# Performance work log

Hardware: AMD Instinct MI355X
Metric: run time of the kernel (lower is better)

Reference implementation:

```python
import jax, jax.numpy as jnp
import numpy as np

DIM = 1024
H = 16
DH = DIM // H
THETA = 10000.0


def _rotary_cos_sin(dtype):
    # Faithful to original: rotary is called on q with shape (B, H, 1, DH) and
    # seq_dim=1, so "positions" are t = arange(num_heads).
    inv_freq = 1.0 / (THETA ** (jnp.arange(0, DH, 2, dtype=jnp.float32) / DH))
    t = jnp.arange(H, dtype=jnp.float32)
    freqs = t[:, None] * inv_freq[None, :]          # (H, DH/2)
    emb = jnp.concatenate([freqs, freqs], axis=-1)   # (H, DH)
    cos = jnp.cos(emb)[None, :, None, :].astype(dtype)  # (1, H, 1, DH)
    sin = jnp.sin(emb)[None, :, None, :].astype(dtype)
    return cos, sin


def _rotate_half(x):
    x1, x2 = x[..., : DH // 2], x[..., DH // 2 :]
    return jnp.concatenate([-x2, x1], axis=-1)


def setup_inputs() -> dict:
    key = jax.random.key(0)
    ks = jax.random.split(key, 6)
    B, N = 16, 4096
    s = 1.0 / np.sqrt(DIM)
    return {
        "x": jax.random.normal(ks[0], (B, N, DIM), dtype=jnp.float32),
        "Wq": jax.random.normal(ks[1], (DIM, DIM), dtype=jnp.float32) * s,
        "Wk": jax.random.normal(ks[2], (DIM, DIM), dtype=jnp.float32) * s,
        "Wv": jax.random.normal(ks[3], (DIM, DIM), dtype=jnp.float32) * s,
        "Wp": jax.random.normal(ks[4], (DIM, DIM), dtype=jnp.float32) * s,
        "bp": jax.random.normal(ks[5], (DIM,), dtype=jnp.float32) * 0.01,
    }


def reference(x, Wq, Wk, Wv, Wp, bp):
    B, N, C = x.shape
    scale = DH ** -0.5
    # projections (weights stored as (in, out); x @ W)
    q = (x[:, :1, :] @ Wq).reshape(B, 1, H, DH).transpose(0, 2, 1, 3)  # (B,H,1,DH)
    k = (x @ Wk).reshape(B, N, H, DH).transpose(0, 2, 1, 3)            # (B,H,N,DH)
    v = (x @ Wv).reshape(B, N, H, DH).transpose(0, 2, 1, 3)            # (B,H,N,DH)
    cos, sin = _rotary_cos_sin(x.dtype)
    q = q * cos + _rotate_half(q) * sin
    k = k * cos + _rotate_half(k) * sin  # broadcasts over N (per original)
    attn = jnp.einsum("bhqd,bhkd->bhqk", q, k) * scale  # (B,H,1,N)
    attn = jax.nn.softmax(attn, axis=-1)
    out = jnp.einsum("bhqk,bhkd->bhqd", attn, v)        # (B,H,1,DH)
    out = out.transpose(0, 2, 1, 3).reshape(B, 1, C)
    return out @ Wp + bp
```

## Files before the change

kernel.cpp:

```cpp
#include <hip/hip_runtime.h>

#define NB 16
#define SEQ 4096
#define DIMC 1024
#define NH 16
#define DH 64
#define NC 64
#define RS 16

#define OFF_Q    0
#define OFF_WTIL 16384
#define OFF_PMAX 278528
#define OFF_LC   294912
#define OFF_E    311296
#define OFF_YOUT 1359872
#define OFF_HO   5554176

__global__ __launch_bounds__(256) void kq(const float* __restrict__ x,
                                          const float* __restrict__ Wq,
                                          float* __restrict__ qws) {
  const int jc = blockIdx.x, b = blockIdx.y, t = threadIdx.x;
  const int d = t & 63, g = t >> 6;
  const int j = jc * 64 + d;
  const float* x0 = x + (size_t)b * SEQ * DIMC;
  __shared__ float red[256];
  float a = 0.f;
  #pragma unroll 8
  for (int c = g * 256; c < g * 256 + 256; ++c)
    a = fmaf(x0[c], Wq[(size_t)c * DIMC + j], a);
  red[t] = a;
  __syncthreads();
  if (t < 64)
    qws[b * DIMC + jc * 64 + t] = red[t] + red[64 + t] + red[128 + t] + red[192 + t];
}

__global__ __launch_bounds__(256) void kw(const float* __restrict__ Wk,
                                          const float* __restrict__ qws,
                                          float* __restrict__ wtil) {
  const int cb = blockIdx.x, b = blockIdx.y, t = threadIdx.x;
  const int w = t >> 6, l = t & 63;
  float4 qreg[4];
  {
    const float4* q4 = (const float4*)(qws + b * DIMC + l * 16);
    #pragma unroll
    for (int i = 0; i < 4; ++i) qreg[i] = q4[i];
  }
  const int h = l >> 2;
  float* wt = wtil + ((size_t)b * NH + h) * DIMC;
  #pragma unroll 4
  for (int i = 0; i < 16; ++i) {
    const int c = cb * 64 + w * 16 + i;
    const float4* row = (const float4*)(Wk + (size_t)c * DIMC) + l * 4;
    float s = 0.f;
    #pragma unroll
    for (int k = 0; k < 4; ++k) {
      float4 rv = row[k];
      s = fmaf(rv.x, qreg[k].x, s); s = fmaf(rv.y, qreg[k].y, s);
      s = fmaf(rv.z, qreg[k].z, s); s = fmaf(rv.w, qreg[k].w, s);
    }
    s += __shfl_xor(s, 1);
    s += __shfl_xor(s, 2);
    if ((l & 3) == 0) wt[c] = s * 0.125f;
  }
}

__global__ __launch_bounds__(256) void kS(const float* __restrict__ x,
                                          const float* __restrict__ wtil,
                                          float* __restrict__ e,
                                          float* __restrict__ pmax,
                                          float* __restrict__ Lc) {
  const int nc = blockIdx.x, b = blockIdx.y, t = threadIdx.x;
  const int w = t >> 6, l = t & 63;
  const int wq = __builtin_amdgcn_readfirstlane(w);

  const float4* xrow = (const float4*)x + ((size_t)b * SEQ + nc * 64 + l) * 256 + wq * 64;
  const float4* wt   = (const float4*)wtil + ((size_t)b * NH) * 256 + wq * 64;

  float acc[16] = {0.f, 0.f, 0.f, 0.f, 0.f, 0.f, 0.f, 0.f,
                   0.f, 0.f, 0.f, 0.f, 0.f, 0.f, 0.f, 0.f};
  for (int k4 = 0; k4 < 64; k4 += 4) {
    float4 xv[4];
    #pragma unroll
    for (int i = 0; i < 4; ++i) xv[i] = xrow[k4 + i];
    #pragma unroll
    for (int h = 0; h < 16; ++h) {
      #pragma unroll
      for (int i = 0; i < 4; ++i) {
        float4 wv = wt[h * 256 + k4 + i];
        acc[h] = fmaf(xv[i].x, wv.x, acc[h]);
        acc[h] = fmaf(xv[i].y, wv.y, acc[h]);
        acc[h] = fmaf(xv[i].z, wv.z, acc[h]);
        acc[h] = fmaf(xv[i].w, wv.w, acc[h]);
      }
    }
  }

  __shared__ float4 part[4][4][64];
  #pragma unroll
  for (int q = 0; q < 4; ++q)
    part[q][w][l] = make_float4(acc[4 * q], acc[4 * q + 1], acc[4 * q + 2], acc[4 * q + 3]);
  __syncthreads();

  float4 va;
  {
    float4 p0 = part[w][0][l], p1 = part[w][1][l], p2 = part[w][2][l], p3 = part[w][3][l];
    va.x = (p0.x + p1.x) + (p2.x + p3.x);
    va.y = (p0.y + p1.y) + (p2.y + p3.y);
    va.z = (p0.z + p1.z) + (p2.z + p3.z);
    va.w = (p0.w + p1.w) + (p2.w + p3.w);
  }

  float4 m4 = va;
  #pragma unroll
  for (int o = 1; o < 64; o <<= 1) {
    m4.x = fmaxf(m4.x, __shfl_xor(m4.x, o)); m4.y = fmaxf(m4.y, __shfl_xor(m4.y, o));
    m4.z = fmaxf(m4.z, __shfl_xor(m4.z, o)); m4.w = fmaxf(m4.w, __shfl_xor(m4.w, o));
  }
  float4 pv;
  pv.x = __expf(va.x - m4.x); pv.y = __expf(va.y - m4.y);
  pv.z = __expf(va.z - m4.z); pv.w = __expf(va.w - m4.w);
  float4 s4 = pv;
  #pragma unroll
  for (int o = 1; o < 64; o <<= 1) {
    s4.x += __shfl_xor(s4.x, o); s4.y += __shfl_xor(s4.y, o);
    s4.z += __shfl_xor(s4.z, o); s4.w += __shfl_xor(s4.w, o);
  }
  ((float4*)e)[((size_t)b * SEQ + nc * 64 + l) * 4 + w] = pv;
  if (l == 0) {
    ((float4*)(pmax + ((size_t)b * NC + nc) * NH))[w] = m4;
    ((float4*)(Lc + ((size_t)b * NC + nc) * NH))[w] = s4;
  }
}

__global__ __launch_bounds__(256) void kY(const float* __restrict__ x,
                                          const float* __restrict__ e,
                                          const float* __restrict__ pmax,
                                          const float* __restrict__ Lc,
                                          float* __restrict__ yout) {
  const int rs = blockIdx.x, b = blockIdx.y, t = threadIdx.x;
  __shared__ float4 sc4[NC][4];
  __shared__ float4 pl[64][4];

  if (t < 64) {
    const int ch = t;
    float scl[16];
    #pragma unroll
    for (int h = 0; h < 16; ++h) {
      float m  = pmax[((size_t)b * NC + ch) * NH + h];
      float lc = Lc[((size_t)b * NC + ch) * NH + h];
      float M = m;
      #pragma unroll
      for (int o = 1; o < 64; o <<= 1) M = fmaxf(M, __shfl_xor(M, o));
      float ex = __expf(m - M);
      float lw = lc * ex;
      #pragma unroll
      for (int o = 1; o < 64; o <<= 1) lw += __shfl_xor(lw, o);
      scl[h] = ex / lw;
    }
    #pragma unroll
    for (int q = 0; q < 4; ++q)
      sc4[ch][q] = make_float4(scl[4 * q], scl[4 * q + 1], scl[4 * q + 2], scl[4 * q + 3]);
  }

  const float4* x4 = (const float4*)x + (size_t)b * SEQ * 256;
  const float4* e4 = (const float4*)e + (size_t)b * SEQ * 4;

  float4 acc[16];
  #pragma unroll
  for (int h = 0; h < 16; ++h) acc[h] = make_float4(0.f, 0.f, 0.f, 0.f);

  for (int c4 = 0; c4 < 4; ++c4) {
    const int ch = rs * 4 + c4;
    __syncthreads();
    {
      const int r = t >> 2, qd = t & 3;
      float4 ev = e4[(size_t)(ch * 64 + r) * 4 + qd];
      float4 s  = sc4[ch][qd];
      pl[r][qd] = make_float4(ev.x * s.x, ev.y * s.y, ev.z * s.z, ev.w * s.w);
    }
    __syncthreads();

    const float4* xc = x4 + (size_t)(ch * 64) * 256;
    for (int r = 0; r < 64; r += 2) {
      float4 xva = xc[(size_t)r * 256 + t];
      float4 xvb = xc[(size_t)(r + 1) * 256 + t];
      float4 a0 = pl[r][0], a1 = pl[r][1], a2 = pl[r][2], a3 = pl[r][3];
      float4 b0 = pl[r + 1][0], b1 = pl[r + 1][1], b2 = pl[r + 1][2], b3 = pl[r + 1][3];
      #define ACC(h, ev, xv) acc[h].x = fmaf(ev, xv.x, acc[h].x); acc[h].y = fmaf(ev, xv.y, acc[h].y); \
                             acc[h].z = fmaf(ev, xv.z, acc[h].z); acc[h].w = fmaf(ev, xv.w, acc[h].w)
      ACC(0, a0.x, xva); ACC(1, a0.y, xva); ACC(2, a0.z, xva); ACC(3, a0.w, xva);
      ACC(4, a1.x, xva); ACC(5, a1.y, xva); ACC(6, a1.z, xva); ACC(7, a1.w, xva);
      ACC(8, a2.x, xva); ACC(9, a2.y, xva); ACC(10, a2.z, xva); ACC(11, a2.w, xva);
      ACC(12, a3.x, xva); ACC(13, a3.y, xva); ACC(14, a3.z, xva); ACC(15, a3.w, xva);
      ACC(0, b0.x, xvb); ACC(1, b0.y, xvb); ACC(2, b0.z, xvb); ACC(3, b0.w, xvb);
      ACC(4, b1.x, xvb); ACC(5, b1.y, xvb); ACC(6, b1.z, xvb); ACC(7, b1.w, xvb);
      ACC(8, b2.x, xvb); ACC(9, b2.y, xvb); ACC(10, b2.z, xvb); ACC(11, b2.w, xvb);
      ACC(12, b3.x, xvb); ACC(13, b3.y, xvb); ACC(14, b3.z, xvb); ACC(15, b3.w, xvb);
      #undef ACC
    }
  }

  float4* yo = (float4*)yout + (((size_t)b * RS + rs) * NH) * 256 + t;
  #pragma unroll
  for (int h = 0; h < 16; ++h) yo[h * 256] = acc[h];
}

__global__ __launch_bounds__(256) void kV(const float* __restrict__ yout,
                                          const float* __restrict__ Wv,
                                          float* __restrict__ ho) {
  const int cq = blockIdx.x, h = blockIdx.y, b = blockIdx.z, t = threadIdx.x;
  __shared__ float ysum[DIMC];
  __shared__ float red[256];
  #pragma unroll
  for (int i = 0; i < 4; ++i) {
    const int c = i * 256 + t;
    float s = 0.f;
    #pragma unroll
    for (int r = 0; r < RS; ++r)
      s += yout[(((size_t)b * RS + r) * NH + h) * DIMC + c];
    ysum[c] = s;
  }
  __syncthreads();
  const int d = t & 15, g = t >> 4;
  float a = 0.f;
  #pragma unroll 8
  for (int i = 0; i < 64; ++i)
    a = fmaf(ysum[g * 64 + i], Wv[(size_t)(g * 64 + i) * DIMC + h * DH + cq * 16 + d], a);
  red[t] = a;
  __syncthreads();
  if (t < 16) {
    float s = 0.f;
    #pragma unroll
    for (int j = 0; j < 16; ++j) s += red[j * 16 + t];
    ho[(size_t)b * DIMC + h * DH + cq * 16 + t] = s;
  }
}

__global__ __launch_bounds__(256) void k_out(const float* __restrict__ ho,
                                             const float* __restrict__ Wp,
                                             const float* __restrict__ bp,
                                             float* __restrict__ out) {
  const int jc = blockIdx.x, b = blockIdx.y, t = threadIdx.x;
  __shared__ float hs[1024];
  __shared__ float red[256];
  for (int i = t; i < 1024; i += 256)
    hs[i] = ho[(size_t)b * DIMC + i];
  __syncthreads();
  const int d = t & 63, g = t >> 6;
  const int j = jc * 64 + d;
  float a = 0.f;
  #pragma unroll 8
  for (int i = g * 256; i < g * 256 + 256; ++i)
    a = fmaf(hs[i], Wp[(size_t)i * DIMC + j], a);
  red[t] = a;
  __syncthreads();
  if (t < 64)
    out[(size_t)b * DIMC + jc * 64 + t] =
        red[t] + red[64 + t] + red[128 + t] + red[192 + t] + bp[jc * 64 + t];
}

extern "C" void kernel_launch(void* const* d_in, const int* in_sizes, int n_in,
                              void* d_out, int out_size, void* d_ws, size_t ws_size,
                              hipStream_t stream) {
  const float* x  = (const float*)d_in[0];
  const float* Wq = (const float*)d_in[1];
  const float* Wk = (const float*)d_in[2];
  const float* Wv = (const float*)d_in[3];
  const float* Wp = (const float*)d_in[4];
  const float* bp = (const float*)d_in[5];
  float* out = (float*)d_out;
  float* ws = (float*)d_ws;

  float* qws  = ws + OFF_Q;
  float* wtil = ws + OFF_WTIL;
  float* pmax = ws + OFF_PMAX;
  float* Lc   = ws + OFF_LC;
  float* e    = ws + OFF_E;
  float* yout = ws + OFF_YOUT;
  float* ho   = ws + OFF_HO;

  kq<<<dim3(16, NB), 256, 0, stream>>>(x, Wq, qws);
  kw<<<dim3(16, NB), 256, 0, stream>>>(Wk, qws, wtil);
  kS<<<dim3(NC, NB), 256, 0, stream>>>(x, wtil, e, pmax, Lc);
  kY<<<dim3(RS, NB), 256, 0, stream>>>(x, e, pmax, Lc, yout);
  kV<<<dim3(4, NH, NB), 256, 0, stream>>>(yout, Wv, ho);
  k_out<<<dim3(16, NB), 256, 0, stream>>>(ho, Wp, bp, out);
}
```

Before: 561.0 us.

## Restructure score kernel to per-wave head groups and double row-split count

The score kernel now has each wave hold the reduced weights for four heads in registers and stream rows of x with coalesced float4 loads. Each row's dot product is reduced with wave-wide shuffles, which replaces the old scheme of splitting the channel dimension across waves and combining partials through shared memory. The weighted-sum kernel doubles its row-split count (RS from 16 to 32) so each block handles two chunks instead of four, giving more blocks and more parallelism at the cost of more partial outputs for kV to sum. The inner accumulation loop is unrolled by four rows, and the workspace offset for the head outputs is moved to fit the larger partial buffer.

```diff
diff --git a/kernel.cpp b/kernel.cpp
--- a/kernel.cpp
+++ b/kernel.cpp
@@ -6,7 +6,7 @@
 #define NH 16
 #define DH 64
 #define NC 64
-#define RS 16
+#define RS 32
 
 #define OFF_Q    0
 #define OFF_WTIL 16384
@@ -14,7 +14,7 @@
 #define OFF_LC   294912
 #define OFF_E    311296
 #define OFF_YOUT 1359872
-#define OFF_HO   5554176
+#define OFF_HO   9748480
 
 __global__ __launch_bounds__(256) void kq(const float* __restrict__ x,
                                           const float* __restrict__ Wq,
@@ -64,6 +64,16 @@
   }
 }
 
+__device__ __forceinline__ float dot16(const float4* xv, const float4* wv) {
+  float s = 0.f;
+  #pragma unroll
+  for (int i = 0; i < 4; ++i) {
+    s = fmaf(xv[i].x, wv[i].x, s); s = fmaf(xv[i].y, wv[i].y, s);
+    s = fmaf(xv[i].z, wv[i].z, s); s = fmaf(xv[i].w, wv[i].w, s);
+  }
+  return s;
+}
+
 __global__ __launch_bounds__(256) void kS(const float* __restrict__ x,
                                           const float* __restrict__ wtil,
                                           float* __restrict__ e,
@@ -71,43 +81,36 @@
                                           float* __restrict__ Lc) {
   const int nc = blockIdx.x, b = blockIdx.y, t = threadIdx.x;
   const int w = t >> 6, l = t & 63;
-  const int wq = __builtin_amdgcn_readfirstlane(w);
-
-  const float4* xrow = (const float4*)x + ((size_t)b * SEQ + nc * 64 + l) * 256 + wq * 64;
-  const float4* wt   = (const float4*)wtil + ((size_t)b * NH) * 256 + wq * 64;
-
-  float acc[16] = {0.f, 0.f, 0.f, 0.f, 0.f, 0.f, 0.f, 0.f,
-                   0.f, 0.f, 0.f, 0.f, 0.f, 0.f, 0.f, 0.f};
-  for (int k4 = 0; k4 < 64; k4 += 4) {
-    float4 xv[4];
-    #pragma unroll
-    for (int i = 0; i < 4; ++i) xv[i] = xrow[k4 + i];
-    #pragma unroll
-    for (int h = 0; h < 16; ++h) {
-      #pragma unroll
-      for (int i = 0; i < 4; ++i) {
-        float4 wv = wt[h * 256 + k4 + i];
-        acc[h] = fmaf(xv[i].x, wv.x, acc[h]);
-        acc[h] = fmaf(xv[i].y, wv.y, acc[h]);
-        acc[h] = fmaf(xv[i].z, wv.z, acc[h]);
-        acc[h] = fmaf(xv[i].w, wv.w, acc[h]);
-      }
-    }
-  }
-
-  __shared__ float4 part[4][4][64];
-  #pragma unroll
-  for (int q = 0; q < 4; ++q)
-    part[q][w][l] = make_float4(acc[4 * q], acc[4 * q + 1], acc[4 * q + 2], acc[4 * q + 3]);
-  __syncthreads();
-
-  float4 va;
-  {
-    float4 p0 = part[w][0][l], p1 = part[w][1][l], p2 = part[w][2][l], p3 = part[w][3][l];
-    va.x = (p0.x + p1.x) + (p2.x + p3.x);
-    va.y = (p0.y + p1.y) + (p2.y + p3.y);
-    va.z = (p0.z + p1.z) + (p2.z + p3.z);
-    va.w = (p0.w + p1.w) + (p2.w + p3.w);
+
+  const float4* wt4 = (const float4*)wtil + ((size_t)b * NH + w * 4) * 256;
+  float4 wv[4][4];
+  #pragma unroll
+  for (int h = 0; h < 4; ++h)
+    #pragma unroll
+    for (int i = 0; i < 4; ++i) wv[h][i] = wt4[h * 256 + i * 64 + l];
+  const float4* x4 = (const float4*)x + ((size_t)b * SEQ + nc * 64) * 256;
+  float4 va = make_float4(0.f, 0.f, 0.f, 0.f);
+
+  for (int r = 0; r < 64; r += 2) {
+    float4 xa[4], xb[4];
+    #pragma unroll
+    for (int i = 0; i < 4; ++i) xa[i] = x4[r * 256 + i * 64 + l];
+    #pragma unroll
+    for (int i = 0; i < 4; ++i) xb[i] = x4[(r + 1) * 256 + i * 64 + l];
+    float4 sa, sb;
+    sa.x = dot16(xa, wv[0]); sa.y = dot16(xa, wv[1]);
+    sa.z = dot16(xa, wv[2]); sa.w = dot16(xa, wv[3]);
+    sb.x = dot16(xb, wv[0]); sb.y = dot16(xb, wv[1]);
+    sb.z = dot16(xb, wv[2]); sb.w = dot16(xb, wv[3]);
+    #pragma unroll
+    for (int o = 1; o < 64; o <<= 1) {
+      sa.x += __shfl_xor(sa.x, o); sa.y += __shfl_xor(sa.y, o);
+      sa.z += __shfl_xor(sa.z, o); sa.w += __shfl_xor(sa.w, o);
+      sb.x += __shfl_xor(sb.x, o); sb.y += __shfl_xor(sb.y, o);
+      sb.z += __shfl_xor(sb.z, o); sb.w += __shfl_xor(sb.w, o);
+    }
+    if (l == r) va = sa;
+    if (l == r + 1) va = sb;
   }
 
   float4 m4 = va;
@@ -169,8 +172,8 @@
   #pragma unroll
   for (int h = 0; h < 16; ++h) acc[h] = make_float4(0.f, 0.f, 0.f, 0.f);
 
-  for (int c4 = 0; c4 < 4; ++c4) {
-    const int ch = rs * 4 + c4;
+  for (int c4 = 0; c4 < 2; ++c4) {
+    const int ch = rs * 2 + c4;
     __syncthreads();
     {
       const int r = t >> 2, qd = t & 3;
@@ -181,22 +184,24 @@
     __syncthreads();
 
     const float4* xc = x4 + (size_t)(ch * 64) * 256;
-    for (int r = 0; r < 64; r += 2) {
-      float4 xva = xc[(size_t)r * 256 + t];
-      float4 xvb = xc[(size_t)(r + 1) * 256 + t];
-      float4 a0 = pl[r][0], a1 = pl[r][1], a2 = pl[r][2], a3 = pl[r][3];
-      float4 b0 = pl[r + 1][0], b1 = pl[r + 1][1], b2 = pl[r + 1][2], b3 = pl[r + 1][3];
-      #define ACC(h, ev, xv) acc[h].x = fmaf(ev, xv.x, acc[h].x); acc[h].y = fmaf(ev, xv.y, acc[h].y); \
-                             acc[h].z = fmaf(ev, xv.z, acc[h].z); acc[h].w = fmaf(ev, xv.w, acc[h].w)
-      ACC(0, a0.x, xva); ACC(1, a0.y, xva); ACC(2, a0.z, xva); ACC(3, a0.w, xva);
-      ACC(4, a1.x, xva); ACC(5, a1.y, xva); ACC(6, a1.z, xva); ACC(7, a1.w, xva);
-      ACC(8, a2.x, xva); ACC(9, a2.y, xva); ACC(10, a2.z, xva); ACC(11, a2.w, xva);
-      ACC(12, a3.x, xva); ACC(13, a3.y, xva); ACC(14, a3.z, xva); ACC(15, a3.w, xva);
-      ACC(0, b0.x, xvb); ACC(1, b0.y, xvb); ACC(2, b0.z, xvb); ACC(3, b0.w, xvb);
-      ACC(4, b1.x, xvb); ACC(5, b1.y, xvb); ACC(6, b1.z, xvb); ACC(7, b1.w, xvb);
-      ACC(8, b2.x, xvb); ACC(9, b2.y, xvb); ACC(10, b2.z, xvb); ACC(11, b2.w, xvb);
-      ACC(12, b3.x, xvb); ACC(13, b3.y, xvb); ACC(14, b3.z, xvb); ACC(15, b3.w, xvb);
-      #undef ACC
+    for (int r = 0; r < 64; r += 4) {
+      float4 xv0 = xc[(size_t)(r + 0) * 256 + t];
+      float4 xv1 = xc[(size_t)(r + 1) * 256 + t];
+      float4 xv2 = xc[(size_t)(r + 2) * 256 + t];
+      float4 xv3 = xc[(size_t)(r + 3) * 256 + t];
+      #pragma unroll
+      for (int rr = 0; rr < 4; ++rr) {
+        float4 xv = (rr == 0) ? xv0 : (rr == 1) ? xv1 : (rr == 2) ? xv2 : xv3;
+        float4 p0 = pl[r + rr][0], p1 = pl[r + rr][1];
+        float4 p2 = pl[r + rr][2], p3 = pl[r + rr][3];
+        #define ACC(h, ev) acc[h].x = fmaf(ev, xv.x, acc[h].x); acc[h].y = fmaf(ev, xv.y, acc[h].y); \
+                           acc[h].z = fmaf(ev, xv.z, acc[h].z); acc[h].w = fmaf(ev, xv.w, acc[h].w)
+        ACC(0, p0.x); ACC(1, p0.y); ACC(2, p0.z); ACC(3, p0.w);
+        ACC(4, p1.x); ACC(5, p1.y); ACC(6, p1.z); ACC(7, p1.w);
+        ACC(8, p2.x); ACC(9, p2.y); ACC(10, p2.z); ACC(11, p2.w);
+        ACC(12, p3.x); ACC(13, p3.y); ACC(14, p3.z); ACC(15, p3.w);
+        #undef ACC
+      }
     }
   }
 
@@ -215,7 +220,7 @@
   for (int i = 0; i < 4; ++i) {
     const int c = i * 256 + t;
     float s = 0.f;
-    #pragma unroll
+    #pragma unroll 8
     for (int r = 0; r < RS; ++r)
       s += yout[(((size_t)b * RS + r) * NH + h) * DIMC + c];
     ysum[c] = s;
```

Result: faster. 527.1 us (-6.0%).
